# Kernel optimization log

Hardware: AMD Instinct MI355X
Metric: run time of the kernel (lower is better)

The kernel has to match this reference:

```python
import jax, jax.numpy as jnp
import numpy as np


def setup_inputs() -> dict:
    key = jax.random.key(0)
    k1, k2 = jax.random.split(key)
    B, H, W, C = 32, 64, 64, 256
    NUM_EMB = 1024
    x = jax.random.normal(k1, (B, H, W, C), dtype=jnp.float32)
    # torch.rand -> uniform [0, 1)
    code_book = jax.random.uniform(k2, (NUM_EMB, C), dtype=jnp.float32)
    return {"x": x, "code_book": code_book}


def reference(x, code_book):
    """VQ: nearest-codebook lookup.

    x: (b, h, w, c) continuous latents ze.
    code_book: (K, c).
    Returns (zq, indices): quantized latents and discrete codes.
    """
    b, h, w, c = x.shape
    flat = x.reshape(-1, c)  # (N, c) with N = b*h*w
    x_sq = jnp.sum(flat * flat, axis=-1, keepdims=True)          # (N, 1)
    e_sq = jnp.sum(code_book * code_book, axis=-1)               # (K,)
    dots = jnp.einsum('nc,kc->nk', flat, code_book)              # (N, K)
    dist = x_sq + e_sq[None, :] - 2.0 * dots                     # (N, K)
    indices = jnp.argmin(dist, axis=-1)                          # (N,)
    zq = jnp.take(code_book, indices, axis=0).reshape(b, h, w, c)
    return zq, indices.reshape(b, h, w)
```

## Files before the change

### kernel.cpp

```cpp
#include <hip/hip_runtime.h>
#include <math.h>


typedef __attribute__((ext_vector_type(8))) short short8;
typedef __attribute__((ext_vector_type(4))) float f32x4;

#define C_DIM 256
#define BM 128

__device__ __forceinline__ unsigned short f2bf(float f) {
    unsigned u = __float_as_uint(f);
    return (unsigned short)((u + 0x7fffu + ((u >> 16) & 1u)) >> 16);
}

__device__ __forceinline__ void gll16(const void* g, void* l) {
    __builtin_amdgcn_global_load_lds(
        (const __attribute__((address_space(1))) unsigned int*)g,
        (__attribute__((address_space(3))) unsigned int*)l, 16, 0, 0);
}

template <bool PLANES>
__global__ __launch_bounds__(256) void vq_prep(
    const float* __restrict__ cb, unsigned short* __restrict__ cbh,
    unsigned short* __restrict__ cbl, float* __restrict__ e2, int K) {
    int wave = threadIdx.x >> 6;
    int lane = threadIdx.x & 63;
    int code = blockIdx.x * 4 + wave;
    if (code >= K) return;
    float4 v = ((const float4*)(cb + (size_t)code * C_DIM))[lane];
    if constexpr (PLANES) {
        unsigned short h[4], l[4];
#pragma unroll
        for (int i = 0; i < 4; ++i) {
            float f = ((const float*)&v)[i];
            unsigned short hh = f2bf(f);
            h[i] = hh;
            l[i] = f2bf(f - __uint_as_float((unsigned)hh << 16));
        }
        *(ushort4*)(cbh + (size_t)code * C_DIM + lane * 4) = make_ushort4(h[0], h[1], h[2], h[3]);
        *(ushort4*)(cbl + (size_t)code * C_DIM + lane * 4) = make_ushort4(l[0], l[1], l[2], l[3]);
    }
    float s = v.x * v.x + v.y * v.y + v.z * v.z + v.w * v.w;
#pragma unroll
    for (int off = 32; off > 0; off >>= 1) s += __shfl_down(s, off, 64);
    if (lane == 0) e2[code] = s;
}

#define STAGE(CN)                                                              \
    {                                                                          \
        const int b_ = (CN) & 1;                                               \
        const int cb0_ = ((CN) >> 2) * 64, db0_ = ((CN) & 3) * 64;             \
        const int cl_ = tid >> 3, g_ = (tid & 7) ^ (cl_ & 7);                  \
        if constexpr (PLANES) {                                                \
            const unsigned short* sh_ = cbh + (size_t)(cb0_ + cl_) * C_DIM + db0_ + g_ * 8; \
            const unsigned short* sl_ = cbl + (size_t)(cb0_ + cl_) * C_DIM + db0_ + g_ * 8; \
            gll16(sh_, smem + b_ * 16384 + w * 1024);                          \
            gll16(sl_, smem + b_ * 16384 + 8192 + w * 1024);                   \
        } else {                                                               \
            const float* sp_ = cb + (size_t)(cb0_ + cl_) * C_DIM + db0_ + g_ * 8; \
            float4 b0_ = ((const float4*)sp_)[0], b1_ = ((const float4*)sp_)[1]; \
            short8 hi_, lo_;                                                   \
            _Pragma("unroll")                                                  \
            for (int i = 0; i < 8; ++i) {                                      \
                float f_ = (i < 4) ? ((const float*)&b0_)[i]                   \
                                   : ((const float*)&b1_)[i - 4];              \
                unsigned short hh_ = f2bf(f_);                                 \
                hi_[i] = (short)hh_;                                           \
                lo_[i] = (short)f2bf(f_ - __uint_as_float((unsigned)hh_ << 16)); \
            }                                                                  \
            *(short8*)(smem + b_ * 16384 + tid * 16) = hi_;                    \
            *(short8*)(smem + b_ * 16384 + 8192 + tid * 16) = lo_;             \
        }                                                                      \
    }

#define LOADB(BH, BL, BUF, KSL)                                                \
    {                                                                          \
        _Pragma("unroll")                                                      \
        for (int nt = 0; nt < 4; ++nt) {                                       \
            int cl_ = nt * 16 + ln;                                            \
            int sl_ = ((KSL) * 4 + q) ^ (cl_ & 7);                             \
            BH[nt] = *(const short8*)(smem + (BUF) * 16384 + cl_ * 128 + sl_ * 16); \
            BL[nt] = *(const short8*)(smem + (BUF) * 16384 + 8192 + cl_ * 128 + sl_ * 16); \
        }                                                                      \
    }

#define MFMA3(AHF, ALF, BH, BL)                                                \
    {                                                                          \
        _Pragma("unroll")                                                      \
        for (int nt = 0; nt < 4; ++nt)                                         \
            acc[nt] = __builtin_amdgcn_mfma_f32_16x16x32_bf16(AHF, BH[nt], acc[nt], 0, 0, 0); \
        _Pragma("unroll")                                                      \
        for (int nt = 0; nt < 4; ++nt)                                         \
            acc[nt] = __builtin_amdgcn_mfma_f32_16x16x32_bf16(ALF, BH[nt], acc[nt], 0, 0, 0); \
        _Pragma("unroll")                                                      \
        for (int nt = 0; nt < 4; ++nt)                                         \
            acc[nt] = __builtin_amdgcn_mfma_f32_16x16x32_bf16(AHF, BL[nt], acc[nt], 0, 0, 0); \
    }

template <bool PLANES>
__global__ __launch_bounds__(512, 2) void vq_main(
    const float* __restrict__ x, const float* __restrict__ cb,
    const unsigned short* __restrict__ cbh, const unsigned short* __restrict__ cbl,
    const float* __restrict__ e2, float* __restrict__ zq, float* __restrict__ idxf,
    int K) {

    __shared__ char smem[32768];

    const int tid = threadIdx.x;
    const int lane = tid & 63;
    const int w = tid >> 6;
    const int ln = lane & 15;
    const int q = lane >> 4;
    const size_t basep = (size_t)blockIdx.x * BM;

    short8 Ah[8], Al[8];
    {
        const float* xr = x + (basep + w * 16 + ln) * C_DIM + q * 8;
#pragma unroll
        for (int ks = 0; ks < 8; ++ks) {
            float4 a0 = ((const float4*)(xr + ks * 32))[0];
            float4 a1 = ((const float4*)(xr + ks * 32))[1];
            short8 hi, lo;
#pragma unroll
            for (int i = 0; i < 8; ++i) {
                float f = (i < 4) ? ((const float*)&a0)[i] : ((const float*)&a1)[i - 4];
                unsigned short hh = f2bf(f);
                hi[i] = (short)hh;
                lo[i] = (short)f2bf(f - __uint_as_float((unsigned)hh << 16));
            }
            Ah[ks] = hi;
            Al[ks] = lo;
        }
    }

    STAGE(0)
    __syncthreads();

    float d1s[4], d2s[4];
    int c1s[4], c2s[4];
#pragma unroll
    for (int r = 0; r < 4; ++r) { d1s[r] = 1e30f; d2s[r] = 1e30f; c1s[r] = 0; c2s[r] = 1; }

    const int ncg = K >> 6;
#pragma unroll 1
    for (int cg = 0; cg < ncg; ++cg) {
        f32x4 acc[4];
#pragma unroll
        for (int nt = 0; nt < 4; ++nt)
#pragma unroll
            for (int r = 0; r < 4; ++r) acc[nt][r] = 0.0f;

        int cnv[4];
        float e2v[4];
#pragma unroll
        for (int nt = 0; nt < 4; ++nt) {
            cnv[nt] = cg * 64 + nt * 16 + ln;
            e2v[nt] = e2[cnv[nt]];
        }

#pragma unroll
        for (int dc = 0; dc < 4; ++dc) {
            const int c = cg * 4 + dc;
            const int buf = dc & 1;
            if (c < 4 * (K >> 6) - 1) {
                STAGE(c + 1)
            }
            short8 Bh[4], Bl[4];
            LOADB(Bh, Bl, buf, 0)
            MFMA3(Ah[2 * dc], Al[2 * dc], Bh, Bl)
            LOADB(Bh, Bl, buf, 1)
            MFMA3(Ah[2 * dc + 1], Al[2 * dc + 1], Bh, Bl)
            __syncthreads();
        }

#pragma unroll
        for (int nt = 0; nt < 4; ++nt)
#pragma unroll
            for (int r = 0; r < 4; ++r) {
                float d = fmaf(-2.0f, acc[nt][r], e2v[nt]);
                int cn = cnv[nt];
                bool lt1 = d < d1s[r];
                bool lt2 = d < d2s[r];
                int tc = lt1 ? c1s[r] : cn;
                c2s[r] = lt2 ? tc : c2s[r];
                c1s[r] = lt1 ? cn : c1s[r];
                d2s[r] = __builtin_amdgcn_fmed3f(d, d1s[r], d2s[r]);
                d1s[r] = fminf(d, d1s[r]);
            }
    }

#pragma unroll
    for (int m = 1; m <= 8; m <<= 1) {
#pragma unroll
        for (int r = 0; r < 4; ++r) {
            float od1 = __shfl_xor(d1s[r], m);
            int oc1 = __shfl_xor(c1s[r], m);
            float od2 = __shfl_xor(d2s[r], m);
            int oc2 = __shfl_xor(c2s[r], m);
            bool t = (od1 < d1s[r]) || (od1 == d1s[r] && oc1 < c1s[r]);
            float hd = t ? d1s[r] : od1;
            int hc = t ? c1s[r] : oc1;
            float nd1 = t ? od1 : d1s[r];
            int nc1 = t ? oc1 : c1s[r];
            bool u = od2 < d2s[r];
            float md = u ? od2 : d2s[r];
            int mc = u ? oc2 : c2s[r];
            bool v2 = (hd < md) || (hd == md && hc < mc);
            d2s[r] = v2 ? hd : md;
            c2s[r] = v2 ? hc : mc;
            d1s[r] = nd1;
            c1s[r] = nc1;
        }
    }

    int* sCand = (int*)smem;
    int* sWin = (int*)(smem + 1024);

    if (ln == 0) {
#pragma unroll
        for (int r = 0; r < 4; ++r) {
            int p = w * 16 + q * 4 + r;
            sCand[p * 2] = c1s[r];
            sCand[p * 2 + 1] = c2s[r];
        }
    }
    __syncthreads();

    if (tid < 2 * BM) {
        int p = tid >> 1;
        int cc = sCand[tid];
        const float4* xr4 = (const float4*)(x + (basep + p) * C_DIM);
        const float4* cr4 = (const float4*)(cb + (size_t)cc * C_DIM);
        float4 s4 = {0.f, 0.f, 0.f, 0.f};
#pragma unroll 8
        for (int j = 0; j < 64; ++j) {
            float4 a = xr4[j], b = cr4[j];
            s4.x = fmaf(a.x, b.x, s4.x);
            s4.y = fmaf(a.y, b.y, s4.y);
            s4.z = fmaf(a.z, b.z, s4.z);
            s4.w = fmaf(a.w, b.w, s4.w);
        }
        float dot = (s4.x + s4.y) + (s4.z + s4.w);
        float d = fmaf(-2.0f, dot, e2[cc]);
        float od = __shfl_xor(d, 1);
        int oc = __shfl_xor(cc, 1);
        int winc = (d < od || (d == od && cc < oc)) ? cc : oc;
        if ((tid & 1) == 0) {
            sWin[p] = winc;
            idxf[basep + p] = (float)winc;
        }
    }
    __syncthreads();

#pragma unroll 2
    for (int pl = 0; pl < 16; ++pl) {
        int p = w * 16 + pl;
        int cc = sWin[p];
        float4 v = ((const float4*)(cb + (size_t)cc * C_DIM))[lane];
        ((float4*)(zq + (basep + p) * C_DIM))[lane] = v;
    }
}

extern "C" void kernel_launch(void* const* d_in, const int* in_sizes, int n_in,
                              void* d_out, int out_size, void* d_ws, size_t ws_size,
                              hipStream_t stream) {
    const float* x = (const float*)d_in[0];
    const float* cb = (const float*)d_in[1];
    int N = in_sizes[0] / C_DIM;
    int K = in_sizes[1] / C_DIM;

    float* zq = (float*)d_out;
    float* idxf = zq + (size_t)N * C_DIM;

    float* e2 = (float*)d_ws;
    unsigned short* cbh = (unsigned short*)((char*)d_ws + 4096);
    unsigned short* cbl = cbh + (size_t)K * C_DIM;
    size_t need = 4096 + (size_t)K * C_DIM * 2 * sizeof(unsigned short);

    if (ws_size >= need) {
        vq_prep<true><<<dim3((K + 3) / 4), dim3(256), 0, stream>>>(cb, cbh, cbl, e2, K);
        vq_main<true><<<dim3(N / BM), dim3(512), 0, stream>>>(x, cb, cbh, cbl, e2, zq, idxf, K);
    } else {
        vq_prep<false><<<dim3((K + 3) / 4), dim3(256), 0, stream>>>(cb, cbh, cbl, e2, K);
        vq_main<false><<<dim3(N / BM), dim3(512), 0, stream>>>(x, cb, cbh, cbl, e2, zq, idxf, K);
    }
}
```

Measured before the change: 454.7 us.

## Stage codebook in 128-wide chunks with two-ahead prefetch and LDS-cached norms

Restructures the codebook pipeline so each stage loads a 64-code by 128-dim chunk (two per code group) instead of 64-dim chunks. Loads are issued two stages ahead, with explicit vmcnt waits and raw barriers in place of a full sync after every chunk. The codebook norms are also copied into LDS once per block rather than read from global memory in each group. The aim is fewer barriers and better hiding of global-load latency. In exchange, shared memory grows to about 68 KB, which may limit occupancy under the two-blocks-per-CU launch bound.

```diff
diff --git a/kernel.cpp b/kernel.cpp
--- a/kernel.cpp
+++ b/kernel.cpp
@@ -49,14 +49,26 @@
 #define STAGE(CN)                                                              \
     {                                                                          \
         const int b_ = (CN) & 1;                                               \
-        const int cb0_ = ((CN) >> 2) * 64, db0_ = ((CN) & 3) * 64;             \
-        const int cl_ = tid >> 3, g_ = (tid & 7) ^ (cl_ & 7);                  \
-        if constexpr (PLANES) {                                                \
+        const int cb0_ = ((CN) >> 1) * 64, db0_ = ((CN) & 1) * 128;            \
+        _Pragma("unroll")                                                      \
+        for (int j = 0; j < 2; ++j) {                                          \
+            const int s_ = j * 512 + tid;                                      \
+            const int cl_ = s_ >> 4, g_ = (s_ & 15) ^ (cl_ & 15);              \
             const unsigned short* sh_ = cbh + (size_t)(cb0_ + cl_) * C_DIM + db0_ + g_ * 8; \
             const unsigned short* sl_ = cbl + (size_t)(cb0_ + cl_) * C_DIM + db0_ + g_ * 8; \
-            gll16(sh_, smem + b_ * 16384 + w * 1024);                          \
-            gll16(sl_, smem + b_ * 16384 + 8192 + w * 1024);                   \
-        } else {                                                               \
+            gll16(sh_, smem + b_ * 32768 + j * 8192 + w * 1024);               \
+            gll16(sl_, smem + b_ * 32768 + 16384 + j * 8192 + w * 1024);       \
+        }                                                                      \
+    }
+
+#define STAGE_F(CN)                                                            \
+    {                                                                          \
+        const int b_ = (CN) & 1;                                               \
+        const int cb0_ = ((CN) >> 1) * 64, db0_ = ((CN) & 1) * 128;            \
+        _Pragma("unroll")                                                      \
+        for (int j = 0; j < 2; ++j) {                                          \
+            const int s_ = j * 512 + tid;                                      \
+            const int cl_ = s_ >> 4, g_ = (s_ & 15) ^ (cl_ & 15);              \
             const float* sp_ = cb + (size_t)(cb0_ + cl_) * C_DIM + db0_ + g_ * 8; \
             float4 b0_ = ((const float4*)sp_)[0], b1_ = ((const float4*)sp_)[1]; \
             short8 hi_, lo_;                                                   \
@@ -68,8 +80,8 @@
                 hi_[i] = (short)hh_;                                           \
                 lo_[i] = (short)f2bf(f_ - __uint_as_float((unsigned)hh_ << 16)); \
             }                                                                  \
-            *(short8*)(smem + b_ * 16384 + tid * 16) = hi_;                    \
-            *(short8*)(smem + b_ * 16384 + 8192 + tid * 16) = lo_;             \
+            *(short8*)(smem + b_ * 32768 + s_ * 16) = hi_;                     \
+            *(short8*)(smem + b_ * 32768 + 16384 + s_ * 16) = lo_;             \
         }                                                                      \
     }
 
@@ -78,9 +90,9 @@
         _Pragma("unroll")                                                      \
         for (int nt = 0; nt < 4; ++nt) {                                       \
             int cl_ = nt * 16 + ln;                                            \
-            int sl_ = ((KSL) * 4 + q) ^ (cl_ & 7);                             \
-            BH[nt] = *(const short8*)(smem + (BUF) * 16384 + cl_ * 128 + sl_ * 16); \
-            BL[nt] = *(const short8*)(smem + (BUF) * 16384 + 8192 + cl_ * 128 + sl_ * 16); \
+            int g_ = ((KSL) * 4 + q) ^ (cl_ & 15);                             \
+            BH[nt] = *(const short8*)(smem + (BUF) * 32768 + cl_ * 256 + g_ * 16); \
+            BL[nt] = *(const short8*)(smem + (BUF) * 32768 + 16384 + cl_ * 256 + g_ * 16); \
         }                                                                      \
     }
 
@@ -95,6 +107,29 @@
         _Pragma("unroll")                                                      \
         for (int nt = 0; nt < 4; ++nt)                                         \
             acc[nt] = __builtin_amdgcn_mfma_f32_16x16x32_bf16(AHF, BL[nt], acc[nt], 0, 0, 0); \
+    }
+
+#define COMPUTE(DC)                                                            \
+    {                                                                          \
+        _Pragma("unroll")                                                      \
+        for (int ksl = 0; ksl < 4; ++ksl) {                                    \
+            short8 Bh[4], Bl[4];                                               \
+            LOADB(Bh, Bl, DC, ksl)                                             \
+            MFMA3(Ah[(DC) * 4 + ksl], Al[(DC) * 4 + ksl], Bh, Bl)              \
+        }                                                                      \
+    }
+
+#define ITER(DC)                                                               \
+    {                                                                          \
+        if (cg * 2 + (DC) + 1 == NC)                                           \
+            asm volatile("s_waitcnt vmcnt(0)" ::: "memory");                   \
+        else                                                                   \
+            asm volatile("s_waitcnt vmcnt(4)" ::: "memory");                   \
+        __builtin_amdgcn_s_barrier();                                          \
+        __builtin_amdgcn_sched_barrier(0);                                     \
+        COMPUTE(DC)                                                            \
+        __builtin_amdgcn_s_barrier();                                          \
+        if (cg * 2 + (DC) + 2 < NC) { STAGE(cg * 2 + (DC) + 2) }               \
     }
 
 template <bool PLANES>
@@ -104,7 +139,7 @@
     const float* __restrict__ e2, float* __restrict__ zq, float* __restrict__ idxf,
     int K) {
 
-    __shared__ char smem[32768];
+    __shared__ char smem[69632];
 
     const int tid = threadIdx.x;
     const int lane = tid & 63;
@@ -112,6 +147,14 @@
     const int ln = lane & 15;
     const int q = lane >> 4;
     const size_t basep = (size_t)blockIdx.x * BM;
+    float* sE2 = (float*)(smem + 65536);
+
+    const int NC = K >> 5;
+
+    if constexpr (PLANES) {
+        STAGE(0)
+        STAGE(1)
+    }
 
     short8 Ah[8], Al[8];
     {
@@ -133,7 +176,8 @@
         }
     }
 
-    STAGE(0)
+    if (tid < (K >> 1)) ((float2*)sE2)[tid] = ((const float2*)e2)[tid];
+
     __syncthreads();
 
     float d1s[4], d2s[4];
@@ -150,27 +194,26 @@
 #pragma unroll
             for (int r = 0; r < 4; ++r) acc[nt][r] = 0.0f;
 
+        if constexpr (PLANES) {
+            ITER(0)
+            ITER(1)
+        } else {
+            __syncthreads();
+            STAGE_F(cg * 2)
+            __syncthreads();
+            COMPUTE(0)
+            __syncthreads();
+            STAGE_F(cg * 2 + 1)
+            __syncthreads();
+            COMPUTE(1)
+        }
+
         int cnv[4];
         float e2v[4];
 #pragma unroll
         for (int nt = 0; nt < 4; ++nt) {
             cnv[nt] = cg * 64 + nt * 16 + ln;
-            e2v[nt] = e2[cnv[nt]];
-        }
-
-#pragma unroll
-        for (int dc = 0; dc < 4; ++dc) {
-            const int c = cg * 4 + dc;
-            const int buf = dc & 1;
-            if (c < 4 * (K >> 6) - 1) {
-                STAGE(c + 1)
-            }
-            short8 Bh[4], Bl[4];
-            LOADB(Bh, Bl, buf, 0)
-            MFMA3(Ah[2 * dc], Al[2 * dc], Bh, Bl)
-            LOADB(Bh, Bl, buf, 1)
-            MFMA3(Ah[2 * dc + 1], Al[2 * dc + 1], Bh, Bl)
-            __syncthreads();
+            e2v[nt] = sE2[cnv[nt]];
         }
 
 #pragma unroll
```

Measured after the change: 458.8 us. About the same (+0.9%).
